# Kernel optimization log

Hardware: AMD Instinct MI355X
Metric: run time of the kernel (lower is better)

## Reference

```python
import jax, jax.numpy as jnp
import numpy as np

B, T, E = 4, 2048, 1024
NH = 16            # num_heads
DH = E // NH       # per-head dim
NE = 2048          # num_experts = block_size (literal constructor wiring)
HID = NH           # expert hidden_dim = num_heads (literal constructor wiring)
EPS = 1e-5


def setup_inputs() -> dict:
    key = jax.random.key(0)
    ks = jax.random.split(key, 12)
    s = 0.02
    return {
        "x": jax.random.normal(ks[0], (B, T, E), jnp.float32),
        "ln1_g": jnp.ones((E,), jnp.float32),
        "ln1_b": jnp.zeros((E,), jnp.float32),
        "ln2_g": jnp.ones((E,), jnp.float32),
        "ln2_b": jnp.zeros((E,), jnp.float32),
        "qkv_w": jax.random.normal(ks[1], (E, 3 * E), jnp.float32) * s,
        "qkv_b": jnp.zeros((3 * E,), jnp.float32),
        "proj_w": jax.random.normal(ks[2], (E, E), jnp.float32) * s,
        "proj_b": jnp.zeros((E,), jnp.float32),
        "gate_w": jax.random.normal(ks[3], (E, NE), jnp.float32) * s,
        "gate_b": jnp.zeros((NE,), jnp.float32),
        "w1": jax.random.normal(ks[4], (NE, E, HID), jnp.float32) * s,
        "b1": jnp.zeros((NE, HID), jnp.float32),
        "w2": jax.random.normal(ks[5], (NE, HID, E), jnp.float32) * s,
        "b2": jnp.zeros((NE, E), jnp.float32),
    }


def _layernorm(x, g, b):
    mu = jnp.mean(x, axis=-1, keepdims=True)
    var = jnp.mean(jnp.square(x - mu), axis=-1, keepdims=True)
    return (x - mu) * jax.lax.rsqrt(var + EPS) * g + b


def _attention(h, qkv_w, qkv_b, proj_w, proj_b):
    qkv = h @ qkv_w + qkv_b                       # [B,T,3E]
    qkv = qkv.reshape(h.shape[0], h.shape[1], 3, NH, DH)
    q, k, v = qkv[:, :, 0], qkv[:, :, 1], qkv[:, :, 2]   # [B,T,NH,DH]
    scores = jnp.einsum('bqhd,bkhd->bhqk', q, k) * (DH ** -0.5)
    causal = jnp.tril(jnp.ones((h.shape[1], h.shape[1]), bool))
    scores = jnp.where(causal, scores, -jnp.inf)
    attn = jax.nn.softmax(scores, axis=-1)
    out = jnp.einsum('bhqk,bkhd->bqhd', attn, v).reshape(h.shape[0], h.shape[1], E)
    return out @ proj_w + proj_b


def _moe(h, gate_w, gate_b, w1, b1, w2, b2):
    # top-1 routing via argmax of gate softmax (== argmax of logits)
    logits = h @ gate_w + gate_b                  # [B,T,NE]
    idx = jnp.argmax(logits, axis=-1)             # [B,T]
    xf = h.reshape(-1, E)                         # [N,E]
    fidx = idx.reshape(-1)                        # [N]
    tw1 = w1[fidx]                                # [N,E,HID]
    tb1 = b1[fidx]                                # [N,HID]
    tw2 = w2[fidx]                                # [N,HID,E]
    tb2 = b2[fidx]                                # [N,E]
    hmid = jax.nn.gelu(jnp.einsum('ne,neh->nh', xf, tw1) + tb1, approximate=False)
    yf = jnp.einsum('nh,nhe->ne', hmid, tw2) + tb2
    return yf.reshape(h.shape)


def reference(x, ln1_g, ln1_b, ln2_g, ln2_b, qkv_w, qkv_b, proj_w, proj_b,
              gate_w, gate_b, w1, b1, w2, b2):
    x = x + _attention(_layernorm(x, ln1_g, ln1_b), qkv_w, qkv_b, proj_w, proj_b)
    x = x + _moe(_layernorm(x, ln2_g, ln2_b), gate_w, gate_b, w1, b1, w2, b2)
    return x
```

## Files before the change

### kernel.cpp

```cpp
#include <hip/hip_runtime.h>
#include <math.h>

#define TOKENS 8192
#define EDIM   1024
#define TSEQ   2048
#define NEXP   2048

typedef __attribute__((ext_vector_type(8))) short short8;
typedef __attribute__((ext_vector_type(4))) float f32x4;

__device__ __forceinline__ short f2bf(float f) {
  union { float f; unsigned u; } c; c.f = f;
  unsigned r = c.u + 0x7fffu + ((c.u >> 16) & 1u);
  return (short)(r >> 16);
}
__device__ __forceinline__ float bf2f(short h) {
  union { unsigned u; float f; } c; c.u = ((unsigned)(unsigned short)h) << 16;
  return c.f;
}
__device__ __forceinline__ void split3(float a, short& p0, short& p1, short& p2) {
  p0 = f2bf(a);
  float r = a - bf2f(p0);
  p1 = f2bf(r);
  p2 = f2bf(r - bf2f(p1));
}
__device__ __forceinline__ void split2(float a, short& p0, short& p1) {
  p0 = f2bf(a);
  p1 = f2bf(a - bf2f(p0));
}

__global__ __launch_bounds__(256) void ln_kernel(const float* __restrict__ x,
    const float* __restrict__ g, const float* __restrict__ b,
    short* __restrict__ obf, float* __restrict__ of32)
{
  const int row = blockIdx.x;
  const int t = threadIdx.x, lane = t & 63, w = t >> 6;
  const float4 v = ((const float4*)(x + (size_t)row * EDIM))[t];
  __shared__ float lds[4];
  float s = v.x + v.y + v.z + v.w;
  #pragma unroll
  for (int m = 32; m >= 1; m >>= 1) s += __shfl_xor(s, m);
  if (lane == 0) lds[w] = s;
  __syncthreads();
  const float mu = (lds[0] + lds[1] + lds[2] + lds[3]) * (1.f / EDIM);
  __syncthreads();
  const float d0 = v.x - mu, d1 = v.y - mu, d2 = v.z - mu, d3 = v.w - mu;
  float sq = d0 * d0 + d1 * d1 + d2 * d2 + d3 * d3;
  #pragma unroll
  for (int m = 32; m >= 1; m >>= 1) sq += __shfl_xor(sq, m);
  if (lane == 0) lds[w] = sq;
  __syncthreads();
  const float var = (lds[0] + lds[1] + lds[2] + lds[3]) * (1.f / EDIM);
  const float rstd = rsqrtf(var + 1e-5f);
  const float4 gg = ((const float4*)g)[t];
  const float4 bb = ((const float4*)b)[t];
  const float y0 = d0 * rstd * gg.x + bb.x;
  const float y1 = d1 * rstd * gg.y + bb.y;
  const float y2 = d2 * rstd * gg.z + bb.z;
  const float y3 = d3 * rstd * gg.w + bb.w;
  if (obf) {
    unsigned long long pk =
        (unsigned long long)(unsigned short)f2bf(y0)
      | ((unsigned long long)(unsigned short)f2bf(y1) << 16)
      | ((unsigned long long)(unsigned short)f2bf(y2) << 32)
      | ((unsigned long long)(unsigned short)f2bf(y3) << 48);
    *(unsigned long long*)(obf + (size_t)row * EDIM + t * 4) = pk;
  }
  ((float4*)(of32 + (size_t)row * EDIM))[t] = make_float4(y0, y1, y2, y3);
}

__global__ __launch_bounds__(256) void wsplit_kernel(const float* __restrict__ W,
    short* __restrict__ Wt, int K, int N)
{
  __shared__ float tile[32][33];
  const int n0 = blockIdx.x * 32, k0 = blockIdx.y * 32;
  const int tx = threadIdx.x & 31, ty = threadIdx.x >> 5;
  #pragma unroll
  for (int i = 0; i < 4; i++)
    tile[ty * 4 + i][tx] = W[(size_t)(k0 + ty * 4 + i) * N + n0 + tx];
  __syncthreads();
  const size_t PS = (size_t)N * K;
  #pragma unroll
  for (int i = 0; i < 4; i++) {
    short p0, p1, p2;
    split3(tile[tx][ty * 4 + i], p0, p1, p2);
    const size_t idx = (size_t)(n0 + ty * 4 + i) * K + k0 + tx;
    Wt[idx] = p0; Wt[PS + idx] = p1; Wt[2 * PS + idx] = p2;
  }
}

__global__ __launch_bounds__(256) void wconv_kernel(const float* __restrict__ W,
    short* __restrict__ Wt, int K, int N)
{
  __shared__ float tile[32][33];
  const int n0 = blockIdx.x * 32, k0 = blockIdx.y * 32;
  const int tx = threadIdx.x & 31, ty = threadIdx.x >> 5;
  #pragma unroll
  for (int i = 0; i < 4; i++)
    tile[ty * 4 + i][tx] = W[(size_t)(k0 + ty * 4 + i) * N + n0 + tx];
  __syncthreads();
  #pragma unroll
  for (int i = 0; i < 4; i++)
    Wt[(size_t)(n0 + ty * 4 + i) * K + k0 + tx] = f2bf(tile[tx][ty * 4 + i]);
}

__global__ __launch_bounds__(256) void asplit_kernel(const float* __restrict__ src,
    short* __restrict__ dst, size_t PS)
{
  const size_t g8 = ((size_t)blockIdx.x * 256 + threadIdx.x) * 8;
  float v[8];
  *(float4*)&v[0] = *(const float4*)(src + g8);
  *(float4*)&v[4] = *(const float4*)(src + g8 + 4);
  short pl[3][8];
  #pragma unroll
  for (int j = 0; j < 8; j++) split3(v[j], pl[0][j], pl[1][j], pl[2][j]);
  *(short8*)(dst + g8)          = *(short8*)&pl[0][0];
  *(short8*)(dst + PS + g8)     = *(short8*)&pl[1][0];
  *(short8*)(dst + 2 * PS + g8) = *(short8*)&pl[2][0];
}

__global__ __launch_bounds__(256) void ksplit_kernel(const float* __restrict__ qkvf,
    short* __restrict__ Kp)
{
  const size_t gid = (size_t)blockIdx.x * 256 + threadIdx.x;
  const int tok = (int)(gid >> 7);
  const int c = (int)(gid & 127) * 8;
  const float* src = qkvf + (size_t)tok * 3072 + 1024 + c;
  float v[8];
  *(float4*)&v[0] = *(const float4*)src;
  *(float4*)&v[4] = *(const float4*)(src + 4);
  short pl[3][8];
  #pragma unroll
  for (int j = 0; j < 8; j++) split3(v[j], pl[0][j], pl[1][j], pl[2][j]);
  const size_t PS = (size_t)TOKENS * EDIM;
  const size_t dst = (size_t)tok * EDIM + c;
  *(short8*)(Kp + dst)          = *(short8*)&pl[0][0];
  *(short8*)(Kp + PS + dst)     = *(short8*)&pl[1][0];
  *(short8*)(Kp + 2 * PS + dst) = *(short8*)&pl[2][0];
}

__global__ __launch_bounds__(256) void vtrans_kernel(const float* __restrict__ qkvf,
    short* __restrict__ Vt)
{
  __shared__ float tile[32][33];
  const int bh = blockIdx.x;
  const int b = bh >> 4, h = bh & 15;
  const int t0 = blockIdx.y * 32;
  const int d0 = blockIdx.z * 32;
  const int tx = threadIdx.x & 31, ty = threadIdx.x >> 5;
  #pragma unroll
  for (int i = 0; i < 4; i++)
    tile[ty * 4 + i][tx] =
        qkvf[(size_t)(b * TSEQ + t0 + ty * 4 + i) * 3072 + 2048 + h * 64 + d0 + tx];
  __syncthreads();
  const size_t PS = (size_t)64 * 64 * TSEQ;
  #pragma unroll
  for (int i = 0; i < 4; i++) {
    short p0, p1, p2;
    split3(tile[tx][ty * 4 + i], p0, p1, p2);
    const size_t idx = (size_t)(bh * 64 + d0 + ty * 4 + i) * TSEQ + t0 + tx;
    Vt[idx] = p0; Vt[PS + idx] = p1; Vt[2 * PS + idx] = p2;
  }
}

__global__ __launch_bounds__(256) void __attribute__((noinline)) gemm_hp_dummy() {}
template<int ADD_RES>
__global__ __launch_bounds__(256) void gemm_hp(const short* __restrict__ Ap, size_t astride,
    const short* __restrict__ Bp, size_t bstride, const float* __restrict__ bias,
    const float* __restrict__ resid, float* __restrict__ outp,
    int M, int N, int K)
{
  __shared__ short As[3][128][32];
  __shared__ short Bs[3][128][32];
  const int m0 = blockIdx.y * 128, n0 = blockIdx.x * 128;
  const int t = threadIdx.x;
  const int lane = t & 63, w = t >> 6;
  const int wm = w >> 1, wn = w & 1;
  const int lo = lane & 15, hi = lane >> 4;
  const int rr = t >> 2;
  const int cj = t & 3;
  const int crw = (rr & 3) ^ ((rr >> 2) & 3);
  const int wc8 = ((cj ^ crw)) * 8;
  const int rc8 = ((hi ^ (lo & 3) ^ ((lo >> 2) & 3))) * 8;
  f32x4 acc[4][4];
  #pragma unroll
  for (int i = 0; i < 4; i++)
    #pragma unroll
    for (int j = 0; j < 4; j++)
      acc[i][j] = (f32x4){0.f, 0.f, 0.f, 0.f};

  for (int k0 = 0; k0 < K; k0 += 32) {
    #pragma unroll
    for (int p = 0; p < 3; p++)
      #pragma unroll
      for (int u = 0; u < 2; u++) {
        *(uint4*)&As[p][u * 64 + rr][wc8] =
            *(const uint4*)(Ap + (size_t)p * astride + (size_t)(m0 + u * 64 + rr) * K + k0 + cj * 8);
        *(uint4*)&Bs[p][u * 64 + rr][wc8] =
            *(const uint4*)(Bp + (size_t)p * bstride + (size_t)(n0 + u * 64 + rr) * K + k0 + cj * 8);
      }
    __syncthreads();
    short8 af[3][4], bf[3][4];
    #pragma unroll
    for (int p = 0; p < 3; p++)
      #pragma unroll
      for (int i = 0; i < 4; i++) {
        af[p][i] = *(const short8*)(&As[p][wm * 64 + i * 16 + lo][rc8]);
        bf[p][i] = *(const short8*)(&Bs[p][wn * 64 + i * 16 + lo][rc8]);
      }
    __builtin_amdgcn_s_setprio(1);
    #pragma unroll
    for (int i = 0; i < 4; i++)
      #pragma unroll
      for (int j = 0; j < 4; j++) {
        acc[i][j] = __builtin_amdgcn_mfma_f32_16x16x32_bf16(af[0][i], bf[0][j], acc[i][j], 0, 0, 0);
        acc[i][j] = __builtin_amdgcn_mfma_f32_16x16x32_bf16(af[0][i], bf[1][j], acc[i][j], 0, 0, 0);
        acc[i][j] = __builtin_amdgcn_mfma_f32_16x16x32_bf16(af[1][i], bf[0][j], acc[i][j], 0, 0, 0);
        acc[i][j] = __builtin_amdgcn_mfma_f32_16x16x32_bf16(af[1][i], bf[1][j], acc[i][j], 0, 0, 0);
        acc[i][j] = __builtin_amdgcn_mfma_f32_16x16x32_bf16(af[0][i], bf[2][j], acc[i][j], 0, 0, 0);
        acc[i][j] = __builtin_amdgcn_mfma_f32_16x16x32_bf16(af[2][i], bf[0][j], acc[i][j], 0, 0, 0);
      }
    __builtin_amdgcn_s_setprio(0);
    __syncthreads();
  }
  #pragma unroll
  for (int i = 0; i < 4; i++)
    #pragma unroll
    for (int j = 0; j < 4; j++)
      #pragma unroll
      for (int r = 0; r < 4; r++) {
        const int gm = m0 + wm * 64 + i * 16 + hi * 4 + r;
        const int gn = n0 + wn * 64 + j * 16 + lo;
        float v = acc[i][j][r] + bias[gn];
        if (ADD_RES) v += resid[(size_t)gm * N + gn];
        outp[(size_t)gm * N + gn] = v;
      }
}

__global__ __launch_bounds__(256) void attn_hp(const float* __restrict__ qkvf,
    const short* __restrict__ Kp, const short* __restrict__ Vt,
    float* __restrict__ attno)
{
  const int bh = blockIdx.x;
  const int b = bh >> 4, h = bh & 15;
  const int qb0 = blockIdx.y * 64;
  const int t = threadIdx.x, lane = t & 63, w = t >> 6;
  const int lo = lane & 15, hi = lane >> 4;
  __shared__ short Ks[3][32][72];
  __shared__ short Vs[3][64][40];
  __shared__ short Ps[2][4][16][40];
  const size_t base = (size_t)b * TSEQ * 3072;
  const size_t PSK = (size_t)TOKENS * EDIM;
  const size_t PSV = (size_t)64 * 64 * TSEQ;
  const int qw0 = qb0 + w * 16;
  short8 qf[3][2];
  #pragma unroll
  for (int c = 0; c < 2; c++) {
    const float* qp = qkvf + base + (size_t)(qw0 + lo) * 3072 + h * 64 + c * 32 + hi * 8;
    float qv[8];
    *(float4*)&qv[0] = *(const float4*)qp;
    *(float4*)&qv[4] = *(const float4*)(qp + 4);
    #pragma unroll
    for (int j = 0; j < 8; j++) {
      short s0, s1, s2;
      split3(qv[j] * 0.125f, s0, s1, s2);
      qf[0][c][j] = s0; qf[1][c][j] = s1; qf[2][c][j] = s2;
    }
  }
  float l_r[4] = {0.f, 0.f, 0.f, 0.f};
  f32x4 o[4];
  #pragma unroll
  for (int nb = 0; nb < 4; nb++) o[nb] = (f32x4){0.f, 0.f, 0.f, 0.f};

  const int key = t >> 3, c0 = (t & 7) * 8;
  const int dv = t >> 2, kc = (t & 3) * 8;
  const short* kbase = Kp + (size_t)(b * TSEQ + key) * EDIM + h * 64 + c0;
  const short* vbase = Vt + (size_t)(bh * 64 + dv) * TSEQ + kc;
  short8 kreg0 = *(const short8*)kbase;
  short8 kreg1 = *(const short8*)(kbase + PSK);
  short8 kreg2 = *(const short8*)(kbase + 2 * PSK);
  short8 vreg0 = *(const short8*)vbase;
  short8 vreg1 = *(const short8*)(vbase + PSV);
  short8 vreg2 = *(const short8*)(vbase + 2 * PSV);

  const int ntiles = 2 * blockIdx.y + 2;
  for (int tile = 0; tile < ntiles; tile++) {
    const int kt0 = tile * 32;
    __syncthreads();
    *(short8*)&Ks[0][key][c0] = kreg0;
    *(short8*)&Ks[1][key][c0] = kreg1;
    *(short8*)&Ks[2][key][c0] = kreg2;
    *(short8*)&Vs[0][dv][kc] = vreg0;
    *(short8*)&Vs[1][dv][kc] = vreg1;
    *(short8*)&Vs[2][dv][kc] = vreg2;
    __syncthreads();
    if (tile + 1 < ntiles) {
      const short* kp = kbase + (size_t)(tile + 1) * 32 * EDIM;
      const short* vp = vbase + (tile + 1) * 32;
      kreg0 = *(const short8*)kp;
      kreg1 = *(const short8*)(kp + PSK);
      kreg2 = *(const short8*)(kp + 2 * PSK);
      vreg0 = *(const short8*)vp;
      vreg1 = *(const short8*)(vp + PSV);
      vreg2 = *(const short8*)(vp + 2 * PSV);
    }
    if (kt0 <= qw0 + 15) {
      f32x4 s[2];
      __builtin_amdgcn_s_setprio(1);
      #pragma unroll
      for (int kb = 0; kb < 2; kb++) {
        f32x4 z = (f32x4){0.f, 0.f, 0.f, 0.f};
        #pragma unroll
        for (int c = 0; c < 2; c++) {
          const short8 kf0 = *(const short8*)(&Ks[0][kb * 16 + lo][c * 32 + hi * 8]);
          const short8 kf1 = *(const short8*)(&Ks[1][kb * 16 + lo][c * 32 + hi * 8]);
          const short8 kf2 = *(const short8*)(&Ks[2][kb * 16 + lo][c * 32 + hi * 8]);
          z = __builtin_amdgcn_mfma_f32_16x16x32_bf16(qf[0][c], kf0, z, 0, 0, 0);
          z = __builtin_amdgcn_mfma_f32_16x16x32_bf16(qf[0][c], kf1, z, 0, 0, 0);
          z = __builtin_amdgcn_mfma_f32_16x16x32_bf16(qf[1][c], kf0, z, 0, 0, 0);
          z = __builtin_amdgcn_mfma_f32_16x16x32_bf16(qf[1][c], kf1, z, 0, 0, 0);
          z = __builtin_amdgcn_mfma_f32_16x16x32_bf16(qf[0][c], kf2, z, 0, 0, 0);
          z = __builtin_amdgcn_mfma_f32_16x16x32_bf16(qf[2][c], kf0, z, 0, 0, 0);
        }
        s[kb] = z;
      }
      __builtin_amdgcn_s_setprio(0);
      #pragma unroll
      for (int r = 0; r < 4; r++) {
        const int qg = qw0 + hi * 4 + r;
        #pragma unroll
        for (int kb = 0; kb < 2; kb++) {
          const int kg = kt0 + kb * 16 + lo;
          float v = s[kb][r];
          v = (kg > qg) ? -1e30f : v;
          const float pv = __expf(v);
          s[kb][r] = pv;
          l_r[r] += pv;
        }
      }
      #pragma unroll
      for (int kb = 0; kb < 2; kb++)
        #pragma unroll
        for (int r = 0; r < 4; r++) {
          short p0, p1;
          split2(s[kb][r], p0, p1);
          Ps[0][w][hi * 4 + r][kb * 16 + lo] = p0;
          Ps[1][w][hi * 4 + r][kb * 16 + lo] = p1;
        }
      __threadfence_block();
      const short8 pf0 = *(const short8*)(&Ps[0][w][lo][hi * 8]);
      const short8 pf1 = *(const short8*)(&Ps[1][w][lo][hi * 8]);
      __builtin_amdgcn_s_setprio(1);
      #pragma unroll
      for (int nb = 0; nb < 4; nb++) {
        const short8 vb0 = *(const short8*)(&Vs[0][nb * 16 + lo][hi * 8]);
        const short8 vb1 = *(const short8*)(&Vs[1][nb * 16 + lo][hi * 8]);
        const short8 vb2 = *(const short8*)(&Vs[2][nb * 16 + lo][hi * 8]);
        o[nb] = __builtin_amdgcn_mfma_f32_16x16x32_bf16(pf0, vb0, o[nb], 0, 0, 0);
        o[nb] = __builtin_amdgcn_mfma_f32_16x16x32_bf16(pf0, vb1, o[nb], 0, 0, 0);
        o[nb] = __builtin_amdgcn_mfma_f32_16x16x32_bf16(pf1, vb0, o[nb], 0, 0, 0);
        o[nb] = __builtin_amdgcn_mfma_f32_16x16x32_bf16(pf1, vb1, o[nb], 0, 0, 0);
        o[nb] = __builtin_amdgcn_mfma_f32_16x16x32_bf16(pf0, vb2, o[nb], 0, 0, 0);
      }
      __builtin_amdgcn_s_setprio(0);
    }
  }
  #pragma unroll
  for (int r = 0; r < 4; r++)
    #pragma unroll
    for (int mm = 8; mm >= 1; mm >>= 1) l_r[r] += __shfl_xor(l_r[r], mm);
  #pragma unroll
  for (int nb = 0; nb < 4; nb++)
    #pragma unroll
    for (int r = 0; r < 4; r++) {
      const int tok = qw0 + hi * 4 + r;
      attno[(size_t)(b * TSEQ + tok) * EDIM + h * 64 + nb * 16 + lo] = o[nb][r] / l_r[r];
    }
}

__global__ __launch_bounds__(256) void gemm_bf16(const short* __restrict__ A,
    const short* __restrict__ Bt, const float* __restrict__ bias,
    float* __restrict__ outp, int M, int N, int K)
{
  __shared__ short As[128][72];
  __shared__ short Bs[128][72];
  const int m0 = blockIdx.y * 128, n0 = blockIdx.x * 128;
  const int t = threadIdx.x;
  const int lane = t & 63, w = t >> 6;
  const int wm = w >> 1, wn = w & 1;
  const int lo = lane & 15, hi = lane >> 4;
  f32x4 acc[4][4];
  #pragma unroll
  for (int i = 0; i < 4; i++)
    #pragma unroll
    for (int j = 0; j < 4; j++)
      acc[i][j] = (f32x4){0.f, 0.f, 0.f, 0.f};
  for (int k0 = 0; k0 < K; k0 += 64) {
    #pragma unroll
    for (int c = 0; c < 4; c++) {
      const int cc = t + 256 * c;
      const int row = cc >> 3, col = (cc & 7) * 8;
      *(uint4*)(&As[row][col]) = *(const uint4*)(A + (size_t)(m0 + row) * K + k0 + col);
      *(uint4*)(&Bs[row][col]) = *(const uint4*)(Bt + (size_t)(n0 + row) * K + k0 + col);
    }
    __syncthreads();
    #pragma unroll
    for (int kk = 0; kk < 2; kk++) {
      short8 af[4], bf[4];
      #pragma unroll
      for (int i = 0; i < 4; i++) {
        af[i] = *(const short8*)(&As[wm * 64 + i * 16 + lo][kk * 32 + hi * 8]);
        bf[i] = *(const short8*)(&Bs[wn * 64 + i * 16 + lo][kk * 32 + hi * 8]);
      }
      #pragma unroll
      for (int i = 0; i < 4; i++)
        #pragma unroll
        for (int j = 0; j < 4; j++)
          acc[i][j] = __builtin_amdgcn_mfma_f32_16x16x32_bf16(af[i], bf[j], acc[i][j], 0, 0, 0);
    }
    __syncthreads();
  }
  #pragma unroll
  for (int i = 0; i < 4; i++)
    #pragma unroll
    for (int j = 0; j < 4; j++)
      #pragma unroll
      for (int r = 0; r < 4; r++) {
        const int gm = m0 + wm * 64 + i * 16 + hi * 4 + r;
        const int gn = n0 + wn * 64 + j * 16 + lo;
        outp[(size_t)gm * N + gn] = acc[i][j][r] + bias[gn];
      }
}

__global__ __launch_bounds__(256) void gate_argmax(const float* __restrict__ logits,
    const float* __restrict__ h2f, const float* __restrict__ gw,
    const float* __restrict__ gb, int* __restrict__ eidx)
{
  const int token = blockIdx.x;
  const int t = threadIdx.x, lane = t & 63, w = t >> 6;
  const float* row = logits + (size_t)token * NEXP;
  float bm = -1e30f;
  #pragma unroll
  for (int c = 0; c < 8; c++) bm = fmaxf(bm, row[t + 256 * c]);
  #pragma unroll
  for (int m = 32; m >= 1; m >>= 1) bm = fmaxf(bm, __shfl_xor(bm, m));
  __shared__ float wred[4];
  __shared__ int cnt;
  __shared__ int cand[16];
  __shared__ float sred[4];
  if (t == 0) cnt = 0;
  if (lane == 0) wred[w] = bm;
  __syncthreads();
  const float maxv = fmaxf(fmaxf(wred[0], wred[1]), fmaxf(wred[2], wred[3]));
  const float thr = maxv - 0.03f;
  #pragma unroll
  for (int c = 0; c < 8; c++) {
    const int e = t + 256 * c;
    if (row[e] > thr) {
      const int p = atomicAdd(&cnt, 1);
      if (p < 16) cand[p] = e;
    }
  }
  __syncthreads();
  const int nc = cnt < 16 ? cnt : 16;
  if (nc == 1) {
    if (t == 0) eidx[token] = cand[0];
    return;
  }
  const float* xr = h2f + (size_t)token * EDIM;
  int best = NEXP; float bs = -1e30f;
  for (int c = 0; c < nc; c++) {
    const int e = cand[c];
    float p = 0.f;
    #pragma unroll
    for (int ii = 0; ii < 4; ii++) {
      const int i = t + 256 * ii;
      p += xr[i] * gw[(size_t)i * NEXP + e];
    }
    #pragma unroll
    for (int m = 32; m >= 1; m >>= 1) p += __shfl_xor(p, m);
    if (lane == 0) sred[w] = p;
    __syncthreads();
    const float s = sred[0] + sred[1] + sred[2] + sred[3] + gb[e];
    if (s > bs || (s == bs && e < best)) { bs = s; best = e; }
    __syncthreads();
  }
  if (t == 0) eidx[token] = best;
}

__global__ __launch_bounds__(256) void moe_kernel(const float* __restrict__ h2f,
    const int* __restrict__ eidx, const float* __restrict__ w1,
    const float* __restrict__ b1, const float* __restrict__ w2,
    const float* __restrict__ b2, float* __restrict__ out)
{
  const int token = blockIdx.x;
  const int t = threadIdx.x, lane = t & 63, w = t >> 6;
  const int e = eidx[token];
  const float* xr = h2f + (size_t)token * EDIM;
  const float* w1e = w1 + (size_t)e * (EDIM * 16);
  float acc[16];
  #pragma unroll
  for (int hh = 0; hh < 16; hh++) acc[hh] = 0.f;
  #pragma unroll
  for (int ii = 0; ii < 4; ii++) {
    const int i = t + 256 * ii;
    const float xi = xr[i];
    const float4* wr = (const float4*)(w1e + (size_t)i * 16);
    const float4 r0 = wr[0], r1 = wr[1], r2 = wr[2], r3 = wr[3];
    acc[0] = fmaf(xi, r0.x, acc[0]);  acc[1] = fmaf(xi, r0.y, acc[1]);
    acc[2] = fmaf(xi, r0.z, acc[2]);  acc[3] = fmaf(xi, r0.w, acc[3]);
    acc[4] = fmaf(xi, r1.x, acc[4]);  acc[5] = fmaf(xi, r1.y, acc[5]);
    acc[6] = fmaf(xi, r1.z, acc[6]);  acc[7] = fmaf(xi, r1.w, acc[7]);
    acc[8] = fmaf(xi, r2.x, acc[8]);  acc[9] = fmaf(xi, r2.y, acc[9]);
    acc[10] = fmaf(xi, r2.z, acc[10]); acc[11] = fmaf(xi, r2.w, acc[11]);
    acc[12] = fmaf(xi, r3.x, acc[12]); acc[13] = fmaf(xi, r3.y, acc[13]);
    acc[14] = fmaf(xi, r3.z, acc[14]); acc[15] = fmaf(xi, r3.w, acc[15]);
  }
  #pragma unroll
  for (int hh = 0; hh < 16; hh++)
    #pragma unroll
    for (int m = 32; m >= 1; m >>= 1) acc[hh] += __shfl_xor(acc[hh], m);
  __shared__ float red[4][16];
  __shared__ float hm[16];
  if (lane == 0) {
    #pragma unroll
    for (int hh = 0; hh < 16; hh++) red[w][hh] = acc[hh];
  }
  __syncthreads();
  if (t < 16) {
    const float s = red[0][t] + red[1][t] + red[2][t] + red[3][t] + b1[(size_t)e * 16 + t];
    hm[t] = 0.5f * s * (1.f + erff(s * 0.70710678118654752f));
  }
  __syncthreads();
  const float* w2e = w2 + (size_t)e * (16 * EDIM);
  float4 y = *(const float4*)(b2 + (size_t)e * EDIM + t * 4);
  const float4 res = *(const float4*)(out + (size_t)token * EDIM + t * 4);
  y.x += res.x; y.y += res.y; y.z += res.z; y.w += res.w;
  #pragma unroll
  for (int hh = 0; hh < 16; hh++) {
    const float hv = hm[hh];
    const float4 wv = *(const float4*)(w2e + (size_t)hh * EDIM + t * 4);
    y.x = fmaf(hv, wv.x, y.x);
    y.y = fmaf(hv, wv.y, y.y);
    y.z = fmaf(hv, wv.z, y.z);
    y.w = fmaf(hv, wv.w, y.w);
  }
  *(float4*)(out + (size_t)token * EDIM + t * 4) = y;
}

extern "C" void kernel_launch(void* const* d_in, const int* in_sizes, int n_in,
                              void* d_out, int out_size, void* d_ws, size_t ws_size,
                              hipStream_t stream) {
  const float* x      = (const float*)d_in[0];
  const float* ln1_g  = (const float*)d_in[1];
  const float* ln1_b  = (const float*)d_in[2];
  const float* ln2_g  = (const float*)d_in[3];
  const float* ln2_b  = (const float*)d_in[4];
  const float* qkv_w  = (const float*)d_in[5];
  const float* qkv_b  = (const float*)d_in[6];
  const float* proj_w = (const float*)d_in[7];
  const float* proj_b = (const float*)d_in[8];
  const float* gate_w = (const float*)d_in[9];
  const float* gate_b = (const float*)d_in[10];
  const float* w1     = (const float*)d_in[11];
  const float* b1     = (const float*)d_in[12];
  const float* w2     = (const float*)d_in[13];
  const float* b2     = (const float*)d_in[14];
  float* out = (float*)d_out;

  char* p = (char*)d_ws;
  short* wTq = (short*)p; p += 3ull * 3072 * 1024 * 2;
  short* wTp = (short*)p; p += 3ull * 1024 * 1024 * 2;
  short* wTg = (short*)p; p += 2048ull * 1024 * 2;
  short* h2  = (short*)p; p += (size_t)TOKENS * EDIM * 2;
  int* eidx  = (int*)p;   p += (size_t)TOKENS * 4;
  p = (char*)(((size_t)p + 255) & ~(size_t)255);
  float* R1  = (float*)p; p += (size_t)TOKENS * EDIM * 4;
  float* R2  = (float*)p; p += (size_t)TOKENS * 3072 * 4;
  short* Kp  = (short*)p; p += 3ull * TOKENS * EDIM * 2;
  short* Vt  = (short*)p; p += 3ull * 64 * 64 * TSEQ * 2;
  float* h1f = R1;
  float* attnof = R1;
  float* h2f = R1;
  float* qkvf = R2;
  float* logits = R2;
  const size_t PSA = (size_t)TOKENS * EDIM;

  wsplit_kernel<<<dim3(3072 / 32, 1024 / 32), 256, 0, stream>>>(qkv_w, wTq, 1024, 3072);
  wsplit_kernel<<<dim3(1024 / 32, 1024 / 32), 256, 0, stream>>>(proj_w, wTp, 1024, 1024);
  wconv_kernel<<<dim3(2048 / 32, 1024 / 32), 256, 0, stream>>>(gate_w, wTg, 1024, 2048);

  ln_kernel<<<TOKENS, 256, 0, stream>>>(x, ln1_g, ln1_b, nullptr, h1f);
  asplit_kernel<<<PSA / 8 / 256, 256, 0, stream>>>(h1f, Kp, PSA);
  gemm_hp<0><<<dim3(3072 / 128, TOKENS / 128), 256, 0, stream>>>(
      Kp, PSA, wTq, (size_t)3072 * 1024, qkv_b, nullptr, qkvf, TOKENS, 3072, 1024);
  ksplit_kernel<<<TOKENS * 128 / 256, 256, 0, stream>>>(qkvf, Kp);
  vtrans_kernel<<<dim3(64, TSEQ / 32, 2), 256, 0, stream>>>(qkvf, Vt);
  attn_hp<<<dim3(64, TSEQ / 64), 256, 0, stream>>>(qkvf, Kp, Vt, attnof);
  asplit_kernel<<<PSA / 8 / 256, 256, 0, stream>>>(attnof, Kp, PSA);
  gemm_hp<1><<<dim3(1024 / 128, TOKENS / 128), 256, 0, stream>>>(
      Kp, PSA, wTp, (size_t)1024 * 1024, proj_b, x, out, TOKENS, 1024, 1024);
  ln_kernel<<<TOKENS, 256, 0, stream>>>(out, ln2_g, ln2_b, h2, h2f);
  gemm_bf16<<<dim3(2048 / 128, TOKENS / 128), 256, 0, stream>>>(
      h2, wTg, gate_b, logits, TOKENS, 2048, 1024);
  gate_argmax<<<TOKENS, 256, 0, stream>>>(logits, h2f, gate_w, gate_b, eidx);
  moe_kernel<<<TOKENS, 256, 0, stream>>>(h2f, eidx, w1, b1, w2, b2, out);
}
```

Measured before the change: 1.251 ms.

## Group tokens by expert to reuse expert weights across tokens in MoE

Adds per-expert token counting in gate_argmax, a prefix scan, and a scatter that builds per-expert token lists. The MoE kernel then runs one block per expert, looping over its assigned tokens so expert weights stay in cache rather than being refetched per token. This reduces redundant weight traffic but adds three small launches and serializes tokens within an expert, which risks imbalance if routing is skewed.

```diff
diff --git a/kernel.cpp b/kernel.cpp
--- a/kernel.cpp
+++ b/kernel.cpp
@@ -163,7 +163,6 @@
   }
 }
 
-__global__ __launch_bounds__(256) void __attribute__((noinline)) gemm_hp_dummy() {}
 template<int ADD_RES>
 __global__ __launch_bounds__(256) void gemm_hp(const short* __restrict__ Ap, size_t astride,
     const short* __restrict__ Bp, size_t bstride, const float* __restrict__ bias,
@@ -432,9 +431,16 @@
       }
 }
 
+__global__ __launch_bounds__(256) void zero_kernel(int* __restrict__ cnt,
+    int* __restrict__ cursor)
+{
+  const int i = blockIdx.x * 256 + threadIdx.x;
+  cnt[i] = 0; cursor[i] = 0;
+}
+
 __global__ __launch_bounds__(256) void gate_argmax(const float* __restrict__ logits,
     const float* __restrict__ h2f, const float* __restrict__ gw,
-    const float* __restrict__ gb, int* __restrict__ eidx)
+    const float* __restrict__ gb, int* __restrict__ eidx, int* __restrict__ ecnt)
 {
   const int token = blockIdx.x;
   const int t = threadIdx.x, lane = t & 63, w = t >> 6;
@@ -464,7 +470,7 @@
   __syncthreads();
   const int nc = cnt < 16 ? cnt : 16;
   if (nc == 1) {
-    if (t == 0) eidx[token] = cand[0];
+    if (t == 0) { eidx[token] = cand[0]; atomicAdd(&ecnt[cand[0]], 1); }
     return;
   }
   const float* xr = h2f + (size_t)token * EDIM;
@@ -485,67 +491,104 @@
     if (s > bs || (s == bs && e < best)) { bs = s; best = e; }
     __syncthreads();
   }
-  if (t == 0) eidx[token] = best;
-}
-
-__global__ __launch_bounds__(256) void moe_kernel(const float* __restrict__ h2f,
-    const int* __restrict__ eidx, const float* __restrict__ w1,
+  if (t == 0) { eidx[token] = best; atomicAdd(&ecnt[best], 1); }
+}
+
+__global__ __launch_bounds__(256) void scan_kernel(const int* __restrict__ cnt,
+    int* __restrict__ off)
+{
+  __shared__ int ws[256];
+  const int t = threadIdx.x;
+  int v[8]; int s = 0;
+  #pragma unroll
+  for (int j = 0; j < 8; j++) { v[j] = s; s += cnt[t * 8 + j]; }
+  ws[t] = s;
+  __syncthreads();
+  for (int d = 1; d < 256; d <<= 1) {
+    int y = (t >= d) ? ws[t - d] : 0;
+    __syncthreads();
+    ws[t] += y;
+    __syncthreads();
+  }
+  const int base = (t > 0) ? ws[t - 1] : 0;
+  #pragma unroll
+  for (int j = 0; j < 8; j++) off[t * 8 + j] = base + v[j];
+}
+
+__global__ __launch_bounds__(256) void scatter_kernel(const int* __restrict__ eidx,
+    const int* __restrict__ off, int* __restrict__ cursor, int* __restrict__ tlist)
+{
+  const int token = blockIdx.x * 256 + threadIdx.x;
+  const int e = eidx[token];
+  const int pos = atomicAdd(&cursor[e], 1);
+  tlist[off[e] + pos] = token;
+}
+
+__global__ __launch_bounds__(256) void moe_apply(const float* __restrict__ h2f,
+    const int* __restrict__ ecnt, const int* __restrict__ off,
+    const int* __restrict__ tlist, const float* __restrict__ w1,
     const float* __restrict__ b1, const float* __restrict__ w2,
     const float* __restrict__ b2, float* __restrict__ out)
 {
-  const int token = blockIdx.x;
+  const int e = blockIdx.x;
+  const int nt = ecnt[e];
+  if (nt == 0) return;
+  const int base = off[e];
   const int t = threadIdx.x, lane = t & 63, w = t >> 6;
-  const int e = eidx[token];
-  const float* xr = h2f + (size_t)token * EDIM;
   const float* w1e = w1 + (size_t)e * (EDIM * 16);
-  float acc[16];
-  #pragma unroll
-  for (int hh = 0; hh < 16; hh++) acc[hh] = 0.f;
-  #pragma unroll
-  for (int ii = 0; ii < 4; ii++) {
-    const int i = t + 256 * ii;
-    const float xi = xr[i];
-    const float4* wr = (const float4*)(w1e + (size_t)i * 16);
-    const float4 r0 = wr[0], r1 = wr[1], r2 = wr[2], r3 = wr[3];
-    acc[0] = fmaf(xi, r0.x, acc[0]);  acc[1] = fmaf(xi, r0.y, acc[1]);
-    acc[2] = fmaf(xi, r0.z, acc[2]);  acc[3] = fmaf(xi, r0.w, acc[3]);
-    acc[4] = fmaf(xi, r1.x, acc[4]);  acc[5] = fmaf(xi, r1.y, acc[5]);
-    acc[6] = fmaf(xi, r1.z, acc[6]);  acc[7] = fmaf(xi, r1.w, acc[7]);
-    acc[8] = fmaf(xi, r2.x, acc[8]);  acc[9] = fmaf(xi, r2.y, acc[9]);
-    acc[10] = fmaf(xi, r2.z, acc[10]); acc[11] = fmaf(xi, r2.w, acc[11]);
-    acc[12] = fmaf(xi, r3.x, acc[12]); acc[13] = fmaf(xi, r3.y, acc[13]);
-    acc[14] = fmaf(xi, r3.z, acc[14]); acc[15] = fmaf(xi, r3.w, acc[15]);
-  }
-  #pragma unroll
-  for (int hh = 0; hh < 16; hh++)
-    #pragma unroll
-    for (int m = 32; m >= 1; m >>= 1) acc[hh] += __shfl_xor(acc[hh], m);
+  const float* w2e = w2 + (size_t)e * (16 * EDIM);
   __shared__ float red[4][16];
   __shared__ float hm[16];
-  if (lane == 0) {
-    #pragma unroll
-    for (int hh = 0; hh < 16; hh++) red[w][hh] = acc[hh];
-  }
-  __syncthreads();
-  if (t < 16) {
-    const float s = red[0][t] + red[1][t] + red[2][t] + red[3][t] + b1[(size_t)e * 16 + t];
-    hm[t] = 0.5f * s * (1.f + erff(s * 0.70710678118654752f));
-  }
-  __syncthreads();
-  const float* w2e = w2 + (size_t)e * (16 * EDIM);
-  float4 y = *(const float4*)(b2 + (size_t)e * EDIM + t * 4);
-  const float4 res = *(const float4*)(out + (size_t)token * EDIM + t * 4);
-  y.x += res.x; y.y += res.y; y.z += res.z; y.w += res.w;
-  #pragma unroll
-  for (int hh = 0; hh < 16; hh++) {
-    const float hv = hm[hh];
-    const float4 wv = *(const float4*)(w2e + (size_t)hh * EDIM + t * 4);
-    y.x = fmaf(hv, wv.x, y.x);
-    y.y = fmaf(hv, wv.y, y.y);
-    y.z = fmaf(hv, wv.z, y.z);
-    y.w = fmaf(hv, wv.w, y.w);
-  }
-  *(float4*)(out + (size_t)token * EDIM + t * 4) = y;
+  for (int it = 0; it < nt; it++) {
+    const int token = tlist[base + it];
+    const float* xr = h2f + (size_t)token * EDIM;
+    float acc[16];
+    #pragma unroll
+    for (int hh = 0; hh < 16; hh++) acc[hh] = 0.f;
+    #pragma unroll
+    for (int ii = 0; ii < 4; ii++) {
+      const int i = t + 256 * ii;
+      const float xi = xr[i];
+      const float4* wr = (const float4*)(w1e + (size_t)i * 16);
+      const float4 r0 = wr[0], r1 = wr[1], r2 = wr[2], r3 = wr[3];
+      acc[0] = fmaf(xi, r0.x, acc[0]);  acc[1] = fmaf(xi, r0.y, acc[1]);
+      acc[2] = fmaf(xi, r0.z, acc[2]);  acc[3] = fmaf(xi, r0.w, acc[3]);
+      acc[4] = fmaf(xi, r1.x, acc[4]);  acc[5] = fmaf(xi, r1.y, acc[5]);
+      acc[6] = fmaf(xi, r1.z, acc[6]);  acc[7] = fmaf(xi, r1.w, acc[7]);
+      acc[8] = fmaf(xi, r2.x, acc[8]);  acc[9] = fmaf(xi, r2.y, acc[9]);
+      acc[10] = fmaf(xi, r2.z, acc[10]); acc[11] = fmaf(xi, r2.w, acc[11]);
+      acc[12] = fmaf(xi, r3.x, acc[12]); acc[13] = fmaf(xi, r3.y, acc[13]);
+      acc[14] = fmaf(xi, r3.z, acc[14]); acc[15] = fmaf(xi, r3.w, acc[15]);
+    }
+    #pragma unroll
+    for (int hh = 0; hh < 16; hh++)
+      #pragma unroll
+      for (int m = 32; m >= 1; m >>= 1) acc[hh] += __shfl_xor(acc[hh], m);
+    if (lane == 0) {
+      #pragma unroll
+      for (int hh = 0; hh < 16; hh++) red[w][hh] = acc[hh];
+    }
+    __syncthreads();
+    if (t < 16) {
+      const float s = red[0][t] + red[1][t] + red[2][t] + red[3][t] + b1[(size_t)e * 16 + t];
+      hm[t] = 0.5f * s * (1.f + erff(s * 0.70710678118654752f));
+    }
+    __syncthreads();
+    float4 y = *(const float4*)(b2 + (size_t)e * EDIM + t * 4);
+    const float4 res = *(const float4*)(out + (size_t)token * EDIM + t * 4);
+    y.x += res.x; y.y += res.y; y.z += res.z; y.w += res.w;
+    #pragma unroll
+    for (int hh = 0; hh < 16; hh++) {
+      const float hv = hm[hh];
+      const float4 wv = *(const float4*)(w2e + (size_t)hh * EDIM + t * 4);
+      y.x = fmaf(hv, wv.x, y.x);
+      y.y = fmaf(hv, wv.y, y.y);
+      y.z = fmaf(hv, wv.z, y.z);
+      y.w = fmaf(hv, wv.w, y.w);
+    }
+    *(float4*)(out + (size_t)token * EDIM + t * 4) = y;
+    __syncthreads();
+  }
 }
 
 extern "C" void kernel_launch(void* const* d_in, const int* in_sizes, int n_in,
@@ -584,6 +627,10 @@
   float* h2f = R1;
   float* qkvf = R2;
   float* logits = R2;
+  int* ecnt  = (int*)Vt;
+  int* eoff  = ecnt + NEXP;
+  int* ecur  = eoff + NEXP;
+  int* tlist = ecur + NEXP;
   const size_t PSA = (size_t)TOKENS * EDIM;
 
   wsplit_kernel<<<dim3(3072 / 32, 1024 / 32), 256, 0, stream>>>(qkv_w, wTq, 1024, 3072);
@@ -603,6 +650,9 @@
   ln_kernel<<<TOKENS, 256, 0, stream>>>(out, ln2_g, ln2_b, h2, h2f);
   gemm_bf16<<<dim3(2048 / 128, TOKENS / 128), 256, 0, stream>>>(
       h2, wTg, gate_b, logits, TOKENS, 2048, 1024);
-  gate_argmax<<<TOKENS, 256, 0, stream>>>(logits, h2f, gate_w, gate_b, eidx);
-  moe_kernel<<<TOKENS, 256, 0, stream>>>(h2f, eidx, w1, b1, w2, b2, out);
-}
+  zero_kernel<<<NEXP / 256, 256, 0, stream>>>(ecnt, ecur);
+  gate_argmax<<<TOKENS, 256, 0, stream>>>(logits, h2f, gate_w, gate_b, eidx, ecnt);
+  scan_kernel<<<1, 256, 0, stream>>>(ecnt, eoff);
+  scatter_kernel<<<TOKENS / 256, 256, 0, stream>>>(eidx, eoff, ecur, tlist);
+  moe_apply<<<NEXP, 256, 0, stream>>>(h2f, ecnt, eoff, tlist, w1, b1, w2, b2, out);
+}
```

Result: faster. 1.161 ms (-7.2%).
